# Optimization experiments

Hardware: AMD Instinct MI355X
Metric: run time of the kernel (lower is better)

## Reference

```python
import jax, jax.numpy as jnp
import numpy as np

B, C, H, W = 16, 256, 56, 56
HEADS = 4
C_OUT = 256
K = 3
SQ = 16  # squeeze_rate (C=256 >= 80, so not halved)
BN_EPS = 1e-5


def setup_inputs() -> dict:
    key = jax.random.key(0)
    ks = jax.random.split(key, 9)
    r = C // SQ
    cper = C_OUT // HEADS
    return {
        "x": jax.random.normal(ks[0], (B, C, H, W), dtype=jnp.float32),
        "bn_gamma": 1.0 + 0.1 * jax.random.normal(ks[1], (C,), dtype=jnp.float32),
        "bn_beta": 0.1 * jax.random.normal(ks[2], (C,), dtype=jnp.float32),
        "bn_mean": 0.1 * jax.random.normal(ks[3], (C,), dtype=jnp.float32),
        "bn_var": 0.5 + jax.random.uniform(ks[4], (C,), dtype=jnp.float32),
        "fc1_w": 0.1 * jax.random.normal(ks[5], (HEADS, r, C), dtype=jnp.float32),
        "fc2_w": 0.1 * jax.random.normal(ks[6], (HEADS, C, r), dtype=jnp.float32),
        "fc2_b": jnp.ones((HEADS, C), dtype=jnp.float32),  # init.constant_(bias, 1.0)
        "conv_w": 0.05 * jax.random.normal(ks[7], (HEADS, cper, C, K, K), dtype=jnp.float32),
        "inactive_channels": 192,
    }


def reference(x, bn_gamma, bn_beta, bn_mean, bn_var, fc1_w, fc2_w, fc2_b, conv_w, inactive_channels):
    b, c, h, w = x.shape
    heads = fc1_w.shape[0]
    # BatchNorm (inference, running stats) + ReLU
    inv = jax.lax.rsqrt(bn_var + BN_EPS)
    xn = jax.nn.relu((x - bn_mean[None, :, None, None]) * (bn_gamma * inv)[None, :, None, None]
                     + bn_beta[None, :, None, None])
    # Global average pool -> [b, c]
    x_avg = xn.mean(axis=(2, 3))
    # Per-head SE gate: relu(fc2(relu(fc1(x_avg))))  -> [heads, b, c]
    y1 = jax.nn.relu(jnp.einsum("bc,hrc->hbr", x_avg, fc1_w))
    mask = jax.nn.relu(jnp.einsum("hbr,hcr->hbc", y1, fc2_w) + fc2_b[:, None, :])
    lasso_loss = mask.mean(axis=(1, 2)).sum()  # sum over heads of per-head mean
    # topk smallest -> threshold; zero out mask values <= k-th smallest (detached cmp)
    mask_d = jax.lax.stop_gradient(mask)
    if inactive_channels > 0:
        neg_vals, _ = jax.lax.top_k(-mask_d, inactive_channels)  # k largest of -mask
        thresh = -neg_vals[..., -1:]  # k-th smallest of mask, [heads, b, 1]
        mask_c = jnp.where(mask_d <= thresh, 0.0, mask)
    else:
        mask_c = mask
    # Apply per-head channel mask and stack heads: [b, heads*c, h, w]
    mc = jnp.transpose(mask_c, (1, 0, 2))  # [b, heads, c]
    x_mask = (xn[:, None, :, :, :] * mc[:, :, :, None, None]).reshape(b, heads * c, h, w)
    # Grouped conv (groups=heads), weight [heads*cper, c, K, K]
    wflat = conv_w.reshape(-1, c, K, K)
    out = jax.lax.conv_general_dilated(
        x_mask, wflat, window_strides=(1, 1), padding=[(1, 1), (1, 1)],
        dimension_numbers=("NCHW", "OIHW", "NCHW"), feature_group_count=heads)
    bo, co, ho, wo = out.shape
    out = out.reshape(bo, heads, co // heads, ho, wo).transpose(0, 2, 1, 3, 4).reshape(bo, co, ho, wo)
    return out, lasso_loss
```

## Files before the change

kernel.cpp:

```cpp
#include <hip/hip_runtime.h>
#include <hip/hip_bf16.h>
#include <math.h>

#define B_     16
#define C_     256
#define H_     56
#define W_     56
#define HEADS_ 4
#define CPER_  64
#define R_     16
#define HW_    (H_*W_)
#define BN_EPS_ 1e-5f

typedef short bf16x8 __attribute__((ext_vector_type(8)));
typedef float f32x4  __attribute__((ext_vector_type(4)));

__device__ inline unsigned short f2bf(float f) {
    unsigned int u = __builtin_bit_cast(unsigned int, f);
    u += 0x7fffu + ((u >> 16) & 1u);
    return (unsigned short)(u >> 16);
}

__global__ __launch_bounds__(256) void k_pool(
    const float* __restrict__ x,
    const float* __restrict__ gamma, const float* __restrict__ beta,
    const float* __restrict__ mean,  const float* __restrict__ var,
    float* __restrict__ xavg)
{
    int wv = threadIdx.x >> 6, ln = threadIdx.x & 63;
    int plane = blockIdx.x * 4 + wv;
    int c = plane & (C_ - 1);
    float s = gamma[c] * rsqrtf(var[c] + BN_EPS_);
    float t = fmaf(-mean[c], s, beta[c]);
    const float4* xp = (const float4*)(x + (size_t)plane * HW_);
    float s0 = 0.f, s1 = 0.f, s2 = 0.f, s3 = 0.f;
    #pragma unroll
    for (int i = 0; i < 3; ++i) {
        float4 a = xp[ln + (i * 4 + 0) * 64];
        float4 b2 = xp[ln + (i * 4 + 1) * 64];
        float4 c2 = xp[ln + (i * 4 + 2) * 64];
        float4 d = xp[ln + (i * 4 + 3) * 64];
        s0 += fmaxf(fmaf(a.x, s, t), 0.f) + fmaxf(fmaf(a.y, s, t), 0.f)
            + fmaxf(fmaf(a.z, s, t), 0.f) + fmaxf(fmaf(a.w, s, t), 0.f);
        s1 += fmaxf(fmaf(b2.x, s, t), 0.f) + fmaxf(fmaf(b2.y, s, t), 0.f)
            + fmaxf(fmaf(b2.z, s, t), 0.f) + fmaxf(fmaf(b2.w, s, t), 0.f);
        s2 += fmaxf(fmaf(c2.x, s, t), 0.f) + fmaxf(fmaf(c2.y, s, t), 0.f)
            + fmaxf(fmaf(c2.z, s, t), 0.f) + fmaxf(fmaf(c2.w, s, t), 0.f);
        s3 += fmaxf(fmaf(d.x, s, t), 0.f) + fmaxf(fmaf(d.y, s, t), 0.f)
            + fmaxf(fmaf(d.z, s, t), 0.f) + fmaxf(fmaf(d.w, s, t), 0.f);
    }
    if (ln < 16) {
        float4 e = xp[768 + ln];
        s0 += fmaxf(fmaf(e.x, s, t), 0.f) + fmaxf(fmaf(e.y, s, t), 0.f)
            + fmaxf(fmaf(e.z, s, t), 0.f) + fmaxf(fmaf(e.w, s, t), 0.f);
    }
    float sum = (s0 + s1) + (s2 + s3);
    for (int off = 32; off; off >>= 1) sum += __shfl_down(sum, off, 64);
    if (ln == 0) xavg[plane] = sum * (1.f / HW_);
}

__global__ __launch_bounds__(256) void k_se_wg(
    const float* __restrict__ xavg,
    const float* __restrict__ fc1, const float* __restrict__ fc2,
    const float* __restrict__ fc2b, const int* __restrict__ kptr,
    const float* __restrict__ convw,
    int* __restrict__ aidx64, float* __restrict__ lasso,
    short* __restrict__ Wc)
{
    int hb = blockIdx.x;
    int j0 = blockIdx.y * 16;
    int h = hb / B_, b = hb - h * B_;
    int tid = threadIdx.x;

    __shared__ float sav[C_], sy1[R_], smask[C_], sred[4], sthr;
    __shared__ int s_ord[C_];
    __shared__ unsigned long long sbal[4];
    __shared__ int s_act[64];
    __shared__ float s_mv[64];
    __shared__ short sO[9 * 1024];

    sav[tid] = xavg[b * C_ + tid];
    __syncthreads();

    if (tid < R_) {
        const float* w = fc1 + (size_t)(h * R_ + tid) * C_;
        float acc = 0.f;
        for (int c2 = 0; c2 < C_; ++c2) acc = fmaf(sav[c2], w[c2], acc);
        sy1[tid] = fmaxf(acc, 0.f);
    }
    __syncthreads();

    const float* w2 = fc2 + (size_t)(h * C_ + tid) * R_;
    float acc = fc2b[h * C_ + tid];
    for (int r = 0; r < R_; ++r) acc = fmaf(sy1[r], w2[r], acc);
    float m = fmaxf(acc, 0.f);
    smask[tid] = m;
    __syncthreads();

    int lane = tid & 63, wv = tid >> 6;
    float ls = m;
    for (int off = 32; off > 0; off >>= 1) ls += __shfl_down(ls, off, 64);
    if (lane == 0) sred[wv] = ls;

    int cl = 0, ce = 0;
    for (int j = 0; j < C_; ++j) {
        float vj = smask[j];
        cl += (vj < m);
        ce += (vj == m);
    }
    if (tid == 0) sthr = -1e30f;
    __syncthreads();
    int k = kptr[0];
    if (k > 0 && cl <= k - 1 && (k - 1) < cl + ce) sthr = m;
    __syncthreads();

    float thr = sthr;
    float mc = (m <= thr) ? 0.f : m;

    bool active = (mc != 0.f);
    unsigned long long bal = __ballot(active);
    if (lane == 0) sbal[wv] = bal;
    __syncthreads();
    int base = 0, total = 0;
    #pragma unroll
    for (int w = 0; w < 4; ++w) {
        int pc = __popcll(sbal[w]);
        if (w < wv) base += pc;
        total += pc;
    }
    if (active)
        s_ord[base + __popcll(bal & ((1ull << lane) - 1ull))] = tid;
    __syncthreads();

    if (tid < 64) {
        int a = (tid < total) ? s_ord[tid] : 0;
        s_act[tid] = a;
        s_mv[tid]  = (tid < total) ? smask[a] : 0.f;
        if (blockIdx.y == 0) aidx64[hb * 64 + tid] = a;
    }
    if (tid == 0 && blockIdx.y == 0)
        atomicAdd(lasso, (sred[0] + sred[1] + sred[2] + sred[3]) * (1.f / (B_ * C_)));
    __syncthreads();

    const float* wsrc = convw + (size_t)h * CPER_ * C_ * 9;
    for (int it = 0; it < 4; ++it) {
        int e = it * 256 + tid;
        int cp = e & 63, jj = e >> 6;
        int j = j0 + jj;
        const float* wp = wsrc + ((size_t)j * C_ + s_act[cp]) * 9;
        float mv = s_mv[cp];
        int slot = (cp + 8 * (j & 7)) & 63;
        #pragma unroll
        for (int t = 0; t < 9; ++t)
            sO[t * 1024 + jj * 64 + slot] = (short)f2bf(wp[t] * mv);
    }
    __syncthreads();
    short* wdst = Wc + (size_t)hb * 9 * 4096 + j0 * 64;
    for (int it = 0; it < 5; ++it) {
        int v = it * 256 + tid;
        if (v < 1152) {
            int t = v >> 7, r8 = v & 127;
            *(bf16x8*)&wdst[t * 4096 + r8 * 8] = *(const bf16x8*)&sO[t * 1024 + r8 * 8];
        }
    }
}

__global__ __launch_bounds__(256) void k_bnc(
    const float* __restrict__ x,
    const float* __restrict__ gamma, const float* __restrict__ beta,
    const float* __restrict__ mean,  const float* __restrict__ var,
    const int* __restrict__ aidx64, short* __restrict__ xc)
{
    int y = blockIdx.x, b = blockIdx.y;
    int tid = threadIdx.x;
    int h = tid >> 6;
    __shared__ __align__(16) unsigned short T[W_ * 256];

    int c = aidx64[(h * B_ + b) * 64 + (tid & 63)];
    float s = gamma[c] * rsqrtf(var[c] + BN_EPS_);
    float t0 = fmaf(-mean[c], s, beta[c]);
    const float* xrow = x + ((size_t)(b * C_ + c)) * HW_ + y * W_;
    #pragma unroll
    for (int f = 0; f < 14; ++f) {
        float4 v = *(const float4*)(xrow + f * 4);
        int px = f * 4;
        T[(px + 0) * 256 + tid] = f2bf(fmaxf(fmaf(v.x, s, t0), 0.f));
        T[(px + 1) * 256 + tid] = f2bf(fmaxf(fmaf(v.y, s, t0), 0.f));
        T[(px + 2) * 256 + tid] = f2bf(fmaxf(fmaf(v.z, s, t0), 0.f));
        T[(px + 3) * 256 + tid] = f2bf(fmaxf(fmaf(v.w, s, t0), 0.f));
    }
    __syncthreads();

    const uint2* Ts = (const uint2*)T;
    uint2* ob = (uint2*)xc;
    #pragma unroll
    for (int it = 0; it < 14; ++it) {
        int e = it * 256 + tid;
        int px = e >> 6, col4 = e & 63;
        int hh = col4 >> 4, cp4 = col4 & 15;
        uint2 v = Ts[px * 64 + col4];
        ob[((size_t)(hh * B_ + b) * HW_ + (size_t)y * W_ + px) * 16 + cp4] = v;
    }
}

__global__ __launch_bounds__(512, 2) void k_conv(
    const short* __restrict__ xc, const short* __restrict__ Wc,
    float* __restrict__ out, int hbhalf)
{
    int g = blockIdx.x;
    int vx = g & 7, r = g >> 3;
    int b14 = r / 14;
    int sub = r - b14 * 14;
    int hb = vx * 8 + hbhalf * 4 + b14;
    int band = sub >> 1, xh = sub & 1;
    int h = hb >> 4, b = hb & 15;
    int tid = threadIdx.x, lane = tid & 63, wv = tid >> 6;
    int m = lane & 15, q = lane >> 4;
    int yrow = band * 8 + wv;
    int xbase = xh * 32;
    int arot = q * 8 + 8 * (m & 7);

    __shared__ short sW[9 * 4096];

    const short* Wh = Wc + (size_t)hb * 9 * 4096;
    const short* xb = xc + (size_t)hb * HW_ * 64 + q * 8;

    bf16x8 bFb[4][2];
    bf16x8 aFb[2][4];

#define LOADB_(kk) { \
        const int t_ = (kk) >> 1, c0_ = ((kk) & 1) * 32; \
        const int dy_ = t_ / 3 - 1, dx_ = t_ % 3 - 1; \
        int gy_ = yrow + dy_; \
        bool ok_ = (unsigned)gy_ < (unsigned)H_; \
        _Pragma("unroll") \
        for (int xt_ = 0; xt_ < 2; ++xt_) { \
            int gx_ = xbase + xt_ * 16 + m + dx_; \
            bf16x8 v_ = {0, 0, 0, 0, 0, 0, 0, 0}; \
            if (ok_ && (unsigned)gx_ < (unsigned)W_) \
                v_ = *(const bf16x8*)(xb + ((size_t)(gy_ * W_ + gx_)) * 64 + c0_); \
            bFb[(kk) & 3][xt_] = v_; \
        } }

#define LOADA_(kk) { \
        const int t_ = (kk) >> 1, c0_ = ((kk) & 1) * 32; \
        const short* sWc_ = sW + t_ * 4096; \
        _Pragma("unroll") \
        for (int jt_ = 0; jt_ < 4; ++jt_) \
            aFb[(kk) & 1][jt_] = *(const bf16x8*)&sWc_[(jt_ * 16 + m) * 64 + ((c0_ + arot) & 63)]; \
        }

    LOADB_(0);
    LOADB_(1);
    LOADB_(2);

    #pragma unroll
    for (int it = 0; it < 9; ++it) {
        int e = it * 512 + tid;
        *(bf16x8*)&sW[e * 8] = *(const bf16x8*)(Wh + e * 8);
    }
    __syncthreads();

    f32x4 acc[4][2];
    #pragma unroll
    for (int i = 0; i < 4; ++i)
        #pragma unroll
        for (int j = 0; j < 2; ++j)
            #pragma unroll
            for (int rr = 0; rr < 4; ++rr) acc[i][j][rr] = 0.f;

    LOADA_(0);

    #pragma unroll
    for (int k = 0; k < 18; ++k) {
        if (k + 3 < 18) LOADB_(k + 3);
        if (k + 1 < 18) LOADA_(k + 1);
        #pragma unroll
        for (int jt = 0; jt < 4; ++jt)
            #pragma unroll
            for (int xt = 0; xt < 2; ++xt)
                acc[jt][xt] = __builtin_amdgcn_mfma_f32_16x16x32_bf16(
                    aFb[k & 1][jt], bFb[k & 3][xt], acc[jt][xt], 0, 0, 0);
    }
#undef LOADB_
#undef LOADA_

    #pragma unroll
    for (int xt = 0; xt < 2; ++xt) {
        int xx = xbase + xt * 16 + m;
        if (xx < W_) {
            #pragma unroll
            for (int jt = 0; jt < 4; ++jt)
                #pragma unroll
                for (int rr = 0; rr < 4; ++rr) {
                    int j = jt * 16 + q * 4 + rr;
                    int oc = j * HEADS_ + h;
                    out[(((size_t)b * C_ + oc) * H_ + yrow) * W_ + xx] = acc[jt][xt][rr];
                }
        }
    }
}

extern "C" void kernel_launch(void* const* d_in, const int* in_sizes, int n_in,
                              void* d_out, int out_size, void* d_ws, size_t ws_size,
                              hipStream_t stream)
{
    const float* x     = (const float*)d_in[0];
    const float* gamma = (const float*)d_in[1];
    const float* beta  = (const float*)d_in[2];
    const float* mean  = (const float*)d_in[3];
    const float* var   = (const float*)d_in[4];
    const float* fc1   = (const float*)d_in[5];
    const float* fc2   = (const float*)d_in[6];
    const float* fc2b  = (const float*)d_in[7];
    const float* convw = (const float*)d_in[8];
    const int*   kptr  = (const int*)d_in[9];

    float* out   = (float*)d_out;
    float* lasso = out + (size_t)B_ * C_ * HW_;

    char* ws = (char*)d_ws;
    size_t off = 0;
    short* xc    = (short*)(ws + off); off += (size_t)HEADS_ * B_ * HW_ * 64 * 2;
    off = (off + 255) & ~(size_t)255;
    float* xavg  = (float*)(ws + off); off += (size_t)B_ * C_ * 4;
    int*   aidx64= (int*)  (ws + off); off += (size_t)HEADS_ * B_ * 64 * 4;
    off = (off + 255) & ~(size_t)255;
    short* Wc    = (short*)(ws + off); off += (size_t)HEADS_ * B_ * 9 * CPER_ * 64 * 2;

    hipMemsetAsync(lasso, 0, 4, stream);

    k_pool<<<B_ * C_ / 4, 256, 0, stream>>>(x, gamma, beta, mean, var, xavg);
    k_se_wg<<<dim3(HEADS_ * B_, 4), 256, 0, stream>>>(xavg, fc1, fc2, fc2b, kptr, convw,
                                                      aidx64, lasso, Wc);
    k_bnc<<<dim3(H_, B_), 256, 0, stream>>>(x, gamma, beta, mean, var, aidx64, xc);
    k_conv<<<448, 512, 0, stream>>>(xc, Wc, out, 0);
    k_conv<<<448, 512, 0, stream>>>(xc, Wc, out, 1);
}
```

Baseline: 187.0 us.

## Widen conv tiles to full rows, merge conv launches, restructure BN gather

The conv kernel now uses 256-thread blocks covering 4 rows by the full 64-wide (padded) row per wave, so each wave computes a 64x64 tile. It also launches once over all head-batch pairs instead of two half launches. The BN/compact kernel now reads every channel's row coalesced into an LDS transpose buffer, then gathers the active channels from LDS, instead of gathering active channels straight from global. The aim is better weight reuse per block, fewer launches and coalesced x reads, at the cost of more accumulator registers, wasted MFMA work on padded columns 56-63, reading all 256 channels, and more LDS weight-load work per block.

```diff
diff --git a/kernel.cpp b/kernel.cpp
--- a/kernel.cpp
+++ b/kernel.cpp
@@ -173,51 +173,57 @@
 {
     int y = blockIdx.x, b = blockIdx.y;
     int tid = threadIdx.x;
-    int h = tid >> 6;
-    __shared__ __align__(16) unsigned short T[W_ * 256];
-
-    int c = aidx64[(h * B_ + b) * 64 + (tid & 63)];
-    float s = gamma[c] * rsqrtf(var[c] + BN_EPS_);
-    float t0 = fmaf(-mean[c], s, beta[c]);
-    const float* xrow = x + ((size_t)(b * C_ + c)) * HW_ + y * W_;
-    #pragma unroll
-    for (int f = 0; f < 14; ++f) {
-        float4 v = *(const float4*)(xrow + f * 4);
-        int px = f * 4;
-        T[(px + 0) * 256 + tid] = f2bf(fmaxf(fmaf(v.x, s, t0), 0.f));
-        T[(px + 1) * 256 + tid] = f2bf(fmaxf(fmaf(v.y, s, t0), 0.f));
-        T[(px + 2) * 256 + tid] = f2bf(fmaxf(fmaf(v.z, s, t0), 0.f));
-        T[(px + 3) * 256 + tid] = f2bf(fmaxf(fmaf(v.w, s, t0), 0.f));
-    }
-    __syncthreads();
-
-    const uint2* Ts = (const uint2*)T;
-    uint2* ob = (uint2*)xc;
-    #pragma unroll
-    for (int it = 0; it < 14; ++it) {
-        int e = it * 256 + tid;
-        int px = e >> 6, col4 = e & 63;
-        int hh = col4 >> 4, cp4 = col4 & 15;
-        uint2 v = Ts[px * 64 + col4];
-        ob[((size_t)(hh * B_ + b) * HW_ + (size_t)y * W_ + px) * 16 + cp4] = v;
-    }
-}
-
-__global__ __launch_bounds__(512, 2) void k_conv(
+    __shared__ unsigned short T[W_ * 258];
+    __shared__ float ss[C_], st[C_];
+    __shared__ short sact[256];
+
+    {
+        float s = gamma[tid] * rsqrtf(var[tid] + BN_EPS_);
+        ss[tid] = s;
+        st[tid] = fmaf(-mean[tid], s, beta[tid]);
+        int h = tid >> 6, cp = tid & 63;
+        sact[tid] = (short)aidx64[(h * B_ + b) * 64 + cp];
+    }
+    __syncthreads();
+
+    const float* xrow = x + (size_t)b * C_ * HW_ + y * W_;
+    for (int i = tid; i < C_ * 14; i += 256) {
+        int c = i / 14, f = i - c * 14;
+        float4 v = *(const float4*)(xrow + (size_t)c * HW_ + f * 4);
+        float s = ss[c], t = st[c];
+        int xb = f * 4;
+        T[(xb + 0) * 258 + c] = f2bf(fmaxf(fmaf(v.x, s, t), 0.f));
+        T[(xb + 1) * 258 + c] = f2bf(fmaxf(fmaf(v.y, s, t), 0.f));
+        T[(xb + 2) * 258 + c] = f2bf(fmaxf(fmaf(v.z, s, t), 0.f));
+        T[(xb + 3) * 258 + c] = f2bf(fmaxf(fmaf(v.w, s, t), 0.f));
+    }
+    __syncthreads();
+
+    unsigned int* ob = (unsigned int*)xc;
+    #pragma unroll
+    for (int h = 0; h < HEADS_; ++h) {
+        size_t obase = ((size_t)(h * B_ + b) * HW_ + (size_t)y * W_) * 32;
+        for (int i = tid; i < W_ * 32; i += 256) {
+            int px = i >> 5, d = i & 31;
+            unsigned int lo = T[px * 258 + sact[h * 64 + 2 * d]];
+            unsigned int hi = T[px * 258 + sact[h * 64 + 2 * d + 1]];
+            ob[obase + i] = lo | (hi << 16);
+        }
+    }
+}
+
+__global__ __launch_bounds__(256, 2) void k_conv(
     const short* __restrict__ xc, const short* __restrict__ Wc,
-    float* __restrict__ out, int hbhalf)
+    float* __restrict__ out)
 {
     int g = blockIdx.x;
     int vx = g & 7, r = g >> 3;
-    int b14 = r / 14;
-    int sub = r - b14 * 14;
-    int hb = vx * 8 + hbhalf * 4 + b14;
-    int band = sub >> 1, xh = sub & 1;
+    int hb = vx * 8 + r / 14;
+    int band = r - (r / 14) * 14;
     int h = hb >> 4, b = hb & 15;
     int tid = threadIdx.x, lane = tid & 63, wv = tid >> 6;
     int m = lane & 15, q = lane >> 4;
-    int yrow = band * 8 + wv;
-    int xbase = xh * 32;
+    int yrow = band * 4 + wv;
     int arot = q * 8 + 8 * (m & 7);
 
     __shared__ short sW[9 * 4096];
@@ -225,7 +231,7 @@
     const short* Wh = Wc + (size_t)hb * 9 * 4096;
     const short* xb = xc + (size_t)hb * HW_ * 64 + q * 8;
 
-    bf16x8 bFb[4][2];
+    bf16x8 bFb[3][4];
     bf16x8 aFb[2][4];
 
 #define LOADB_(kk) { \
@@ -234,12 +240,12 @@
         int gy_ = yrow + dy_; \
         bool ok_ = (unsigned)gy_ < (unsigned)H_; \
         _Pragma("unroll") \
-        for (int xt_ = 0; xt_ < 2; ++xt_) { \
-            int gx_ = xbase + xt_ * 16 + m + dx_; \
+        for (int xt_ = 0; xt_ < 4; ++xt_) { \
+            int gx_ = xt_ * 16 + m + dx_; \
             bf16x8 v_ = {0, 0, 0, 0, 0, 0, 0, 0}; \
             if (ok_ && (unsigned)gx_ < (unsigned)W_) \
                 v_ = *(const bf16x8*)(xb + ((size_t)(gy_ * W_ + gx_)) * 64 + c0_); \
-            bFb[(kk) & 3][xt_] = v_; \
+            bFb[(kk) % 3][xt_] = v_; \
         } }
 
 #define LOADA_(kk) { \
@@ -247,25 +253,24 @@
         const short* sWc_ = sW + t_ * 4096; \
         _Pragma("unroll") \
         for (int jt_ = 0; jt_ < 4; ++jt_) \
-            aFb[(kk) & 1][jt_] = *(const bf16x8*)&sWc_[(jt_ * 16 + m) * 64 + ((c0_ + arot) & 63)]; \
+            aFb[(kk) % 2][jt_] = *(const bf16x8*)&sWc_[(jt_ * 16 + m) * 64 + ((c0_ + arot) & 63)]; \
         }
 
     LOADB_(0);
     LOADB_(1);
-    LOADB_(2);
-
-    #pragma unroll
-    for (int it = 0; it < 9; ++it) {
-        int e = it * 512 + tid;
+
+    #pragma unroll
+    for (int it = 0; it < 18; ++it) {
+        int e = it * 256 + tid;
         *(bf16x8*)&sW[e * 8] = *(const bf16x8*)(Wh + e * 8);
     }
     __syncthreads();
 
-    f32x4 acc[4][2];
+    f32x4 acc[4][4];
     #pragma unroll
     for (int i = 0; i < 4; ++i)
         #pragma unroll
-        for (int j = 0; j < 2; ++j)
+        for (int j = 0; j < 4; ++j)
             #pragma unroll
             for (int rr = 0; rr < 4; ++rr) acc[i][j][rr] = 0.f;
 
@@ -273,21 +278,21 @@
 
     #pragma unroll
     for (int k = 0; k < 18; ++k) {
-        if (k + 3 < 18) LOADB_(k + 3);
+        if (k + 2 < 18) LOADB_(k + 2);
         if (k + 1 < 18) LOADA_(k + 1);
         #pragma unroll
         for (int jt = 0; jt < 4; ++jt)
             #pragma unroll
-            for (int xt = 0; xt < 2; ++xt)
+            for (int xt = 0; xt < 4; ++xt)
                 acc[jt][xt] = __builtin_amdgcn_mfma_f32_16x16x32_bf16(
-                    aFb[k & 1][jt], bFb[k & 3][xt], acc[jt][xt], 0, 0, 0);
+                    aFb[k % 2][jt], bFb[k % 3][xt], acc[jt][xt], 0, 0, 0);
     }
 #undef LOADB_
 #undef LOADA_
 
     #pragma unroll
-    for (int xt = 0; xt < 2; ++xt) {
-        int xx = xbase + xt * 16 + m;
+    for (int xt = 0; xt < 4; ++xt) {
+        int xx = xt * 16 + m;
         if (xx < W_) {
             #pragma unroll
             for (int jt = 0; jt < 4; ++jt)
@@ -334,6 +339,5 @@
     k_se_wg<<<dim3(HEADS_ * B_, 4), 256, 0, stream>>>(xavg, fc1, fc2, fc2b, kptr, convw,
                                                       aidx64, lasso, Wc);
     k_bnc<<<dim3(H_, B_), 256, 0, stream>>>(x, gamma, beta, mean, var, aidx64, xc);
-    k_conv<<<448, 512, 0, stream>>>(xc, Wc, out, 0);
-    k_conv<<<448, 512, 0, stream>>>(xc, Wc, out, 1);
-}
+    k_conv<<<HEADS_ * B_ * (H_ / 4), 256, 0, stream>>>(xc, Wc, out);
+}
```

Result: faster. 181.4 us (-3.0%).
